# Kernel tuning notes

Hardware: AMD Instinct MI355X
Metric: run time of the kernel (lower is better)

## Reference

```python
import jax, jax.numpy as jnp
import numpy as np

NUM_HEADS = 32
HEAD_DIM = 64  # C = 3 * NUM_HEADS * HEAD_DIM = 6144
SCALE = NUM_HEADS ** (-0.5)


def setup_inputs() -> dict:
    key = jax.random.key(0)
    B, N, C = 4, 4096, 3 * NUM_HEADS * HEAD_DIM
    x = jax.random.normal(key, (B, N, C), dtype=jnp.float32)
    return {"x": x}


def reference(x):
    B, N, C = x.shape
    # (B, N, 3, H, d) -> (3, B, H, N, d)
    qkv = x.reshape(B, N, 3, NUM_HEADS, HEAD_DIM).transpose(2, 0, 3, 1, 4)
    q, k, v = qkv[0], qkv[1], qkv[2]
    q = q * SCALE
    # kv = k^T @ v : (B, H, d, d)
    kv = jnp.einsum('bhnd,bhne->bhde', k, v)
    kv = jax.nn.softmax(kv, axis=-1)  # dropout p=0.0 -> identity
    # attn = q @ kv^T : (B, H, N, d)
    attn = jnp.einsum('bhnd,bhed->bhne', q, kv)
    # (B, H, N, d) -> (B, N, H*d)
    out = attn.transpose(0, 2, 1, 3).reshape(B, N, NUM_HEADS * HEAD_DIM)
    return out
```

## Files before the change

### kernel.cpp

```cpp
#include <hip/hip_runtime.h>
#include <math.h>


#define NN 4096
#define CC 6144
#define QSCALE 0.17677669529663687f
#define NCHUNK 8

typedef __attribute__((ext_vector_type(8))) short bf16x8;
typedef __attribute__((ext_vector_type(4))) float f32x4;

static __device__ __forceinline__ unsigned short f2bf(float f) {
  unsigned u = __float_as_uint(f);
  u = (u + 0x7FFFu + ((u >> 16) & 1u)) >> 16;
  return (unsigned short)u;
}

__global__ __launch_bounds__(256, 4) void k1_kv_accum(const float* __restrict__ x,
                                                      float* __restrict__ ws1) {
  __shared__ float lds[2][4096];

  const int bid = blockIdx.x;
  const int bh = bid >> 3;
  const int chunk = bid & (NCHUNK - 1);
  const int b = bh >> 5, h = bh & 31;
  const int t = threadIdx.x;
  const int lane = t & 63;
  const int w = t >> 6;

  const long long row0 = (long long)b * NN + (long long)chunk * 512;
  const float* kbase = x + row0 * CC + 2048 + h * 64;
  const float* kl = kbase + (lane & 3) * CC + (lane >> 2) + w * 16;
  const float* vl = kl + 2048;

#define K1_STAGE(sb, bbv)                                                                 \
  do {                                                                                    \
    const float* kp_ = kl + (sb) * 32 * CC;                                               \
    const float* vp_ = vl + (sb) * 32 * CC;                                               \
    _Pragma("unroll") for (int r_ = 0; r_ < 2; ++r_)                                      \
    _Pragma("unroll") for (int sub_ = 0; sub_ < 4; ++sub_) {                              \
      const int ro_ = (sub_ * 8 + r_ * 4) * CC;                                           \
      const int li_ = w * 512 + r_ * 256 + sub_ * 64;                                     \
      __builtin_amdgcn_global_load_lds(                                                   \
          (const __attribute__((address_space(1))) void*)(kp_ + ro_),                     \
          (__attribute__((address_space(3))) void*)&lds[(bbv)][li_], 4, 0, 0);            \
      __builtin_amdgcn_global_load_lds(                                                   \
          (const __attribute__((address_space(1))) void*)(vp_ + ro_),                     \
          (__attribute__((address_space(3))) void*)&lds[(bbv)][2048 + li_], 4, 0, 0);     \
    }                                                                                     \
  } while (0)

#define K1_FRAG(bbv, baseidx, hi8, lo8)                                                   \
  do {                                                                                    \
    const float4 f0_ = *(const float4*)&lds[(bbv)][(baseidx) + lane * 4];                 \
    const float4 f1_ = *(const float4*)&lds[(bbv)][(baseidx) + 256 + lane * 4];           \
    const float ff_[8] = {f0_.x, f0_.y, f0_.z, f0_.w, f1_.x, f1_.y, f1_.z, f1_.w};        \
    _Pragma("unroll") for (int e_ = 0; e_ < 8; ++e_) {                                    \
      const unsigned u_ = __float_as_uint(ff_[e_]);                                       \
      hi8[e_] = (short)(u_ >> 16);       \
      const float lof_ = ff_[e_] - __uint_as_float(u_ & 0xFFFF0000u);                     \
      lo8[e_] = (short)(__float_as_uint(lof_) >> 16);                                     \
    }                                                                                     \
  } while (0)

  f32x4 acc[2][2];
#pragma unroll
  for (int i2 = 0; i2 < 2; ++i2)
#pragma unroll
    for (int j2 = 0; j2 < 2; ++j2) acc[i2][j2] = (f32x4){0.f, 0.f, 0.f, 0.f};

  const int mt0 = (w & 1) * 2;
  const int nt0 = (w >> 1) * 2;

  K1_STAGE(0, 0);
  asm volatile("s_waitcnt vmcnt(0)" ::: "memory");
  __syncthreads();

  for (int s = 0; s < 16; ++s) {
    const int bb = s & 1;
    if (s + 1 < 16) K1_STAGE(s + 1, bb ^ 1);

    bf16x8 ah[2], al[2], bh8[2], bl8[2];
#pragma unroll
    for (int i2 = 0; i2 < 2; ++i2) K1_FRAG(bb, (mt0 + i2) * 512, ah[i2], al[i2]);
#pragma unroll
    for (int j2 = 0; j2 < 2; ++j2) K1_FRAG(bb, 2048 + (nt0 + j2) * 512, bh8[j2], bl8[j2]);

#pragma unroll
    for (int i2 = 0; i2 < 2; ++i2)
#pragma unroll
      for (int j2 = 0; j2 < 2; ++j2) {
        acc[i2][j2] = __builtin_amdgcn_mfma_f32_16x16x32_bf16(ah[i2], bh8[j2], acc[i2][j2], 0, 0, 0);
        acc[i2][j2] = __builtin_amdgcn_mfma_f32_16x16x32_bf16(ah[i2], bl8[j2], acc[i2][j2], 0, 0, 0);
        acc[i2][j2] = __builtin_amdgcn_mfma_f32_16x16x32_bf16(al[i2], bh8[j2], acc[i2][j2], 0, 0, 0);
      }

    if (s + 1 < 16) {
      asm volatile("s_waitcnt vmcnt(0)" ::: "memory");
      __syncthreads();
    }
  }

  float* dst = ws1 + (long long)bid * 4096;
  const int g = lane >> 4, cl = lane & 15;
#pragma unroll
  for (int i2 = 0; i2 < 2; ++i2)
#pragma unroll
    for (int j2 = 0; j2 < 2; ++j2)
#pragma unroll
      for (int r = 0; r < 4; ++r)
        dst[((mt0 + i2) * 16 + g * 4 + r) * 64 + (nt0 + j2) * 16 + cl] = acc[i2][j2][r];
}

__global__ __launch_bounds__(256) void k2_softmax(const float* __restrict__ ws1,
                                                  unsigned short* __restrict__ ws2bf) {
  const int bh = blockIdx.x;
  __shared__ float Cs[64 * 65];
  __shared__ float Ss[64 * 65];
  const int t = threadIdx.x;
  const float* src = ws1 + (long long)bh * NCHUNK * 4096;
  for (int s0 = t; s0 < 1024; s0 += 256) {
    float4 sum = {0.f, 0.f, 0.f, 0.f};
#pragma unroll
    for (int c = 0; c < NCHUNK; ++c) {
      const float4 f = *(const float4*)&src[c * 4096 + s0 * 4];
      sum.x += f.x; sum.y += f.y; sum.z += f.z; sum.w += f.w;
    }
    const float se[4] = {sum.x, sum.y, sum.z, sum.w};
#pragma unroll
    for (int e = 0; e < 4; ++e) {
      const int idx = s0 * 4 + e;
      Cs[(idx >> 6) * 65 + (idx & 63)] = se[e];
    }
  }
  __syncthreads();
  if (t < 64) {
    const int a = t;
    float m = -3.0e38f;
    for (int c = 0; c < 64; ++c) m = fmaxf(m, Cs[a * 65 + c]);
    float sum = 0.f;
    for (int c = 0; c < 64; ++c) {
      const float e = expf(Cs[a * 65 + c] - m);
      Ss[a * 65 + c] = e;
      sum += e;
    }
    const float inv = QSCALE / sum;
    for (int c = 0; c < 64; ++c) Ss[a * 65 + c] *= inv;
  }
  __syncthreads();
  unsigned short* dst = ws2bf + (long long)bh * 4096;
  for (int idx = t; idx < 4096; idx += 256) {
    const int j = idx >> 6;
    const int i = idx & 63;
    dst[idx] = f2bf(Ss[j * 65 + i]);
  }
}

__global__ __launch_bounds__(256) void k3_apply(const float* __restrict__ x,
                                                const unsigned short* __restrict__ ws2bf,
                                                float* __restrict__ out) {
  const int bid = blockIdx.x;
  const int bh = bid >> 5;
  const int tile = bid & 31;
  const int b = bh >> 5, h = bh & 31;
  const int t = threadIdx.x;
  const int lane = t & 63;
  const int w = t >> 6;
  const int bn = lane & 15;
  const int g = lane >> 4;

  const unsigned short* mb = ws2bf + (long long)bh * 4096;
  bf16x8 afr[4][2];
#pragma unroll
  for (int mt = 0; mt < 4; ++mt)
#pragma unroll
    for (int kc = 0; kc < 2; ++kc)
      afr[mt][kc] = *(const bf16x8*)(mb + (mt * 16 + bn) * 64 + kc * 32 + g * 8);

  const float* qb = x + ((long long)b * NN + tile * 128) * CC + h * 64;
  bf16x8 bfr[2][2];
#pragma unroll
  for (int u = 0; u < 2; ++u) {
    const int nt = w * 2 + u;
#pragma unroll
    for (int kc = 0; kc < 2; ++kc) {
      const float* p = qb + (long long)(nt * 16 + bn) * CC + kc * 32 + g * 8;
      const float4 f0 = *(const float4*)p;
      const float4 f1 = *(const float4*)(p + 4);
      bf16x8 r;
      r[0] = (short)f2bf(f0.x); r[1] = (short)f2bf(f0.y);
      r[2] = (short)f2bf(f0.z); r[3] = (short)f2bf(f0.w);
      r[4] = (short)f2bf(f1.x); r[5] = (short)f2bf(f1.y);
      r[6] = (short)f2bf(f1.z); r[7] = (short)f2bf(f1.w);
      bfr[u][kc] = r;
    }
  }

  f32x4 acc[2][4];
#pragma unroll
  for (int u = 0; u < 2; ++u)
#pragma unroll
    for (int mt = 0; mt < 4; ++mt) acc[u][mt] = (f32x4){0.f, 0.f, 0.f, 0.f};

#pragma unroll
  for (int kc = 0; kc < 2; ++kc)
#pragma unroll
    for (int u = 0; u < 2; ++u)
#pragma unroll
      for (int mt = 0; mt < 4; ++mt)
        acc[u][mt] = __builtin_amdgcn_mfma_f32_16x16x32_bf16(afr[mt][kc], bfr[u][kc],
                                                             acc[u][mt], 0, 0, 0);

  const long long rowg = (long long)b * NN + tile * 128;
#pragma unroll
  for (int u = 0; u < 2; ++u) {
    const int nt = w * 2 + u;
    const long long r = rowg + nt * 16 + bn;
#pragma unroll
    for (int mt = 0; mt < 4; ++mt) {
      float* op = out + r * 2048 + h * 64 + mt * 16 + g * 4;
      const float4 o = {acc[u][mt][0], acc[u][mt][1], acc[u][mt][2], acc[u][mt][3]};
      *(float4*)op = o;
    }
  }
}

extern "C" void kernel_launch(void* const* d_in, const int* in_sizes, int n_in,
                              void* d_out, int out_size, void* d_ws, size_t ws_size,
                              hipStream_t stream) {
  const float* x = (const float*)d_in[0];
  float* out = (float*)d_out;
  float* ws1 = (float*)d_ws;
  unsigned short* ws2bf = (unsigned short*)(ws1 + (size_t)128 * NCHUNK * 4096);

  k1_kv_accum<<<128 * NCHUNK, 256, 0, stream>>>(x, ws1);
  k2_softmax<<<128, 256, 0, stream>>>(ws1, ws2bf);
  k3_apply<<<128 * 32, 256, 0, stream>>>(x, ws2bf, out);
}
```

Before: 148.9 us.

## Fuse softmax into kv kernel via last-block ticket and retile apply kernel

The softmax stage moves into the kv-accumulation kernel: each chunk block takes an atomic ticket, and the last block for each (b,h) reduces the partial sums, applies softmax and writes the bf16 matrix. This removes one kernel launch and its serial gap, at the cost of a memset and a tail in which 128 blocks run the softmax. The apply kernel is also retiled so each block handles 16 rows across all 32 heads, with 8 heads per wave, which gives contiguous output rows but fewer blocks (1024) and more per-thread work. Fusion only happens when the workspace is large enough to hold the counters.

```diff
diff --git a/kernel.cpp b/kernel.cpp
--- a/kernel.cpp
+++ b/kernel.cpp
@@ -16,9 +16,14 @@
   return (unsigned short)u;
 }
 
-__global__ __launch_bounds__(256, 4) void k1_kv_accum(const float* __restrict__ x,
-                                                      float* __restrict__ ws1) {
-  __shared__ float lds[2][4096];
+__global__ __launch_bounds__(256, 4) void k1_fused(const float* __restrict__ x,
+                                                   float* __restrict__ ws1,
+                                                   unsigned short* __restrict__ ws2bf,
+                                                   unsigned int* __restrict__ cnt,
+                                                   const int fused) {
+  __shared__ float smem[8320];
+  __shared__ unsigned int ticket_s;
+  float(*lds)[4096] = (float(*)[4096])smem;
 
   const int bid = blockIdx.x;
   const int bh = bid >> 3;
@@ -102,14 +107,63 @@
   }
 
   float* dst = ws1 + (long long)bid * 4096;
-  const int g = lane >> 4, cl = lane & 15;
-#pragma unroll
-  for (int i2 = 0; i2 < 2; ++i2)
-#pragma unroll
-    for (int j2 = 0; j2 < 2; ++j2)
-#pragma unroll
-      for (int r = 0; r < 4; ++r)
-        dst[((mt0 + i2) * 16 + g * 4 + r) * 64 + (nt0 + j2) * 16 + cl] = acc[i2][j2][r];
+  {
+    const int g = lane >> 4, cl = lane & 15;
+#pragma unroll
+    for (int i2 = 0; i2 < 2; ++i2)
+#pragma unroll
+      for (int j2 = 0; j2 < 2; ++j2)
+#pragma unroll
+        for (int r = 0; r < 4; ++r)
+          dst[((mt0 + i2) * 16 + g * 4 + r) * 64 + (nt0 + j2) * 16 + cl] = acc[i2][j2][r];
+  }
+
+  if (!fused) return;
+
+  __threadfence();
+  if (t == 0) ticket_s = atomicAdd(&cnt[bh], 1u);
+  __syncthreads();
+  if (ticket_s != NCHUNK - 1) return;
+  __threadfence();
+
+  float* Cs = smem;
+  float* Ss = smem + 4160;
+  const float* src = ws1 + (long long)bh * NCHUNK * 4096;
+  for (int s0 = t; s0 < 1024; s0 += 256) {
+    float4 sum = {0.f, 0.f, 0.f, 0.f};
+#pragma unroll
+    for (int c = 0; c < NCHUNK; ++c) {
+      const float4 f = *(const float4*)&src[c * 4096 + s0 * 4];
+      sum.x += f.x; sum.y += f.y; sum.z += f.z; sum.w += f.w;
+    }
+    const float se[4] = {sum.x, sum.y, sum.z, sum.w};
+#pragma unroll
+    for (int e = 0; e < 4; ++e) {
+      const int idx = s0 * 4 + e;
+      Cs[(idx >> 6) * 65 + (idx & 63)] = se[e];
+    }
+  }
+  __syncthreads();
+  if (t < 64) {
+    const int a = t;
+    float m = -3.0e38f;
+    for (int c = 0; c < 64; ++c) m = fmaxf(m, Cs[a * 65 + c]);
+    float sum = 0.f;
+    for (int c = 0; c < 64; ++c) {
+      const float e = expf(Cs[a * 65 + c] - m);
+      Ss[a * 65 + c] = e;
+      sum += e;
+    }
+    const float inv = QSCALE / sum;
+    for (int c = 0; c < 64; ++c) Ss[a * 65 + c] *= inv;
+  }
+  __syncthreads();
+  unsigned short* dstb = ws2bf + (long long)bh * 4096;
+  for (int idx = t; idx < 4096; idx += 256) {
+    const int j = idx >> 6;
+    const int i = idx & 63;
+    dstb[idx] = f2bf(Ss[j * 65 + i]);
+  }
 }
 
 __global__ __launch_bounds__(256) void k2_softmax(const float* __restrict__ ws1,
@@ -160,31 +214,35 @@
                                                 const unsigned short* __restrict__ ws2bf,
                                                 float* __restrict__ out) {
   const int bid = blockIdx.x;
-  const int bh = bid >> 5;
-  const int tile = bid & 31;
-  const int b = bh >> 5, h = bh & 31;
+  const int b = bid >> 8;
+  const int tile = bid & 255;
   const int t = threadIdx.x;
   const int lane = t & 63;
   const int w = t >> 6;
   const int bn = lane & 15;
   const int g = lane >> 4;
 
-  const unsigned short* mb = ws2bf + (long long)bh * 4096;
-  bf16x8 afr[4][2];
-#pragma unroll
-  for (int mt = 0; mt < 4; ++mt)
-#pragma unroll
-    for (int kc = 0; kc < 2; ++kc)
-      afr[mt][kc] = *(const bf16x8*)(mb + (mt * 16 + bn) * 64 + kc * 32 + g * 8);
-
-  const float* qb = x + ((long long)b * NN + tile * 128) * CC + h * 64;
-  bf16x8 bfr[2][2];
-#pragma unroll
-  for (int u = 0; u < 2; ++u) {
-    const int nt = w * 2 + u;
+  const long long row = (long long)b * NN + tile * 16 + bn;
+  const float* qrow = x + row * CC;
+  float* orow = out + row * 2048;
+  const unsigned short* sbase = ws2bf + (long long)b * 32 * 4096;
+
+#pragma unroll 2
+  for (int hh = 0; hh < 8; ++hh) {
+    const int h = w * 8 + hh;
+    const unsigned short* mb = sbase + h * 4096;
+
+    bf16x8 afr[4][2];
+#pragma unroll
+    for (int mt = 0; mt < 4; ++mt)
+#pragma unroll
+      for (int kc = 0; kc < 2; ++kc)
+        afr[mt][kc] = *(const bf16x8*)(mb + (mt * 16 + bn) * 64 + kc * 32 + g * 8);
+
+    bf16x8 bfr[2];
 #pragma unroll
     for (int kc = 0; kc < 2; ++kc) {
-      const float* p = qb + (long long)(nt * 16 + bn) * CC + kc * 32 + g * 8;
+      const float* p = qrow + h * 64 + kc * 32 + g * 8;
       const float4 f0 = *(const float4*)p;
       const float4 f1 = *(const float4*)(p + 4);
       bf16x8 r;
@@ -192,35 +250,22 @@
       r[2] = (short)f2bf(f0.z); r[3] = (short)f2bf(f0.w);
       r[4] = (short)f2bf(f1.x); r[5] = (short)f2bf(f1.y);
       r[6] = (short)f2bf(f1.z); r[7] = (short)f2bf(f1.w);
-      bfr[u][kc] = r;
-    }
-  }
-
-  f32x4 acc[2][4];
-#pragma unroll
-  for (int u = 0; u < 2; ++u)
-#pragma unroll
-    for (int mt = 0; mt < 4; ++mt) acc[u][mt] = (f32x4){0.f, 0.f, 0.f, 0.f};
-
-#pragma unroll
-  for (int kc = 0; kc < 2; ++kc)
-#pragma unroll
-    for (int u = 0; u < 2; ++u)
+      bfr[kc] = r;
+    }
+
+    f32x4 acc[4];
+#pragma unroll
+    for (int mt = 0; mt < 4; ++mt) acc[mt] = (f32x4){0.f, 0.f, 0.f, 0.f};
+#pragma unroll
+    for (int kc = 0; kc < 2; ++kc)
 #pragma unroll
       for (int mt = 0; mt < 4; ++mt)
-        acc[u][mt] = __builtin_amdgcn_mfma_f32_16x16x32_bf16(afr[mt][kc], bfr[u][kc],
-                                                             acc[u][mt], 0, 0, 0);
-
-  const long long rowg = (long long)b * NN + tile * 128;
-#pragma unroll
-  for (int u = 0; u < 2; ++u) {
-    const int nt = w * 2 + u;
-    const long long r = rowg + nt * 16 + bn;
+        acc[mt] = __builtin_amdgcn_mfma_f32_16x16x32_bf16(afr[mt][kc], bfr[kc], acc[mt], 0, 0, 0);
+
 #pragma unroll
     for (int mt = 0; mt < 4; ++mt) {
-      float* op = out + r * 2048 + h * 64 + mt * 16 + g * 4;
-      const float4 o = {acc[u][mt][0], acc[u][mt][1], acc[u][mt][2], acc[u][mt][3]};
-      *(float4*)op = o;
+      const float4 o = {acc[mt][0], acc[mt][1], acc[mt][2], acc[mt][3]};
+      *(float4*)&orow[h * 64 + mt * 16 + g * 4] = o;
     }
   }
 }
@@ -232,8 +277,16 @@
   float* out = (float*)d_out;
   float* ws1 = (float*)d_ws;
   unsigned short* ws2bf = (unsigned short*)(ws1 + (size_t)128 * NCHUNK * 4096);
-
-  k1_kv_accum<<<128 * NCHUNK, 256, 0, stream>>>(x, ws1);
-  k2_softmax<<<128, 256, 0, stream>>>(ws1, ws2bf);
-  k3_apply<<<128 * 32, 256, 0, stream>>>(x, ws2bf, out);
-}
+  const size_t base_bytes = (size_t)128 * NCHUNK * 4096 * 4 + (size_t)128 * 4096 * 2;
+  unsigned int* cnt = (unsigned int*)((char*)d_ws + base_bytes);
+  const bool can_fuse = ws_size >= base_bytes + 128 * sizeof(unsigned int);
+
+  if (can_fuse) {
+    hipMemsetAsync(cnt, 0, 128 * sizeof(unsigned int), stream);
+    k1_fused<<<128 * NCHUNK, 256, 0, stream>>>(x, ws1, ws2bf, cnt, 1);
+  } else {
+    k1_fused<<<128 * NCHUNK, 256, 0, stream>>>(x, ws1, ws2bf, cnt, 0);
+    k2_softmax<<<128, 256, 0, stream>>>(ws1, ws2bf);
+  }
+  k3_apply<<<1024, 256, 0, stream>>>(x, ws2bf, out);
+}
```

After: 394.4 us. +164.9%, slower.

## Remap apply kernel so each block covers all heads for 16 rows

Applied to the files above, without the earlier changes.

The apply kernel's work mapping changes from one block per (batch, head, 128-row tile) to one block per (batch, 16-row tile) covering all 32 heads, with each wave looping over 8 heads. Each block now reads and writes whole contiguous row segments of q and out, which should improve DRAM locality, and the grid shrinks from 4096 to 1024 blocks. In exchange, every block reloads the softmaxed kv matrix for all 32 heads, about 256KB of bf16 per block, which puts more pressure on L2. Per-wave parallelism also falls, since only one 16-row tile is in flight per head iteration.

```diff
diff --git a/kernel.cpp b/kernel.cpp
--- a/kernel.cpp
+++ b/kernel.cpp
@@ -160,31 +160,35 @@
                                                 const unsigned short* __restrict__ ws2bf,
                                                 float* __restrict__ out) {
   const int bid = blockIdx.x;
-  const int bh = bid >> 5;
-  const int tile = bid & 31;
-  const int b = bh >> 5, h = bh & 31;
+  const int b = bid >> 8;
+  const int tile = bid & 255;
   const int t = threadIdx.x;
   const int lane = t & 63;
   const int w = t >> 6;
   const int bn = lane & 15;
   const int g = lane >> 4;
 
-  const unsigned short* mb = ws2bf + (long long)bh * 4096;
-  bf16x8 afr[4][2];
-#pragma unroll
-  for (int mt = 0; mt < 4; ++mt)
-#pragma unroll
-    for (int kc = 0; kc < 2; ++kc)
-      afr[mt][kc] = *(const bf16x8*)(mb + (mt * 16 + bn) * 64 + kc * 32 + g * 8);
-
-  const float* qb = x + ((long long)b * NN + tile * 128) * CC + h * 64;
-  bf16x8 bfr[2][2];
-#pragma unroll
-  for (int u = 0; u < 2; ++u) {
-    const int nt = w * 2 + u;
+  const long long row = (long long)b * NN + tile * 16 + bn;
+  const float* qrow = x + row * CC;
+  float* orow = out + row * 2048;
+  const unsigned short* sbase = ws2bf + (long long)b * 32 * 4096;
+
+#pragma unroll 2
+  for (int hh = 0; hh < 8; ++hh) {
+    const int h = w * 8 + hh;
+    const unsigned short* mb = sbase + h * 4096;
+
+    bf16x8 afr[4][2];
+#pragma unroll
+    for (int mt = 0; mt < 4; ++mt)
+#pragma unroll
+      for (int kc = 0; kc < 2; ++kc)
+        afr[mt][kc] = *(const bf16x8*)(mb + (mt * 16 + bn) * 64 + kc * 32 + g * 8);
+
+    bf16x8 bfr[2];
 #pragma unroll
     for (int kc = 0; kc < 2; ++kc) {
-      const float* p = qb + (long long)(nt * 16 + bn) * CC + kc * 32 + g * 8;
+      const float* p = qrow + h * 64 + kc * 32 + g * 8;
       const float4 f0 = *(const float4*)p;
       const float4 f1 = *(const float4*)(p + 4);
       bf16x8 r;
@@ -192,35 +196,22 @@
       r[2] = (short)f2bf(f0.z); r[3] = (short)f2bf(f0.w);
       r[4] = (short)f2bf(f1.x); r[5] = (short)f2bf(f1.y);
       r[6] = (short)f2bf(f1.z); r[7] = (short)f2bf(f1.w);
-      bfr[u][kc] = r;
-    }
-  }
-
-  f32x4 acc[2][4];
-#pragma unroll
-  for (int u = 0; u < 2; ++u)
-#pragma unroll
-    for (int mt = 0; mt < 4; ++mt) acc[u][mt] = (f32x4){0.f, 0.f, 0.f, 0.f};
-
-#pragma unroll
-  for (int kc = 0; kc < 2; ++kc)
-#pragma unroll
-    for (int u = 0; u < 2; ++u)
+      bfr[kc] = r;
+    }
+
+    f32x4 acc[4];
+#pragma unroll
+    for (int mt = 0; mt < 4; ++mt) acc[mt] = (f32x4){0.f, 0.f, 0.f, 0.f};
+#pragma unroll
+    for (int kc = 0; kc < 2; ++kc)
 #pragma unroll
       for (int mt = 0; mt < 4; ++mt)
-        acc[u][mt] = __builtin_amdgcn_mfma_f32_16x16x32_bf16(afr[mt][kc], bfr[u][kc],
-                                                             acc[u][mt], 0, 0, 0);
-
-  const long long rowg = (long long)b * NN + tile * 128;
-#pragma unroll
-  for (int u = 0; u < 2; ++u) {
-    const int nt = w * 2 + u;
-    const long long r = rowg + nt * 16 + bn;
+        acc[mt] = __builtin_amdgcn_mfma_f32_16x16x32_bf16(afr[mt][kc], bfr[kc], acc[mt], 0, 0, 0);
+
 #pragma unroll
     for (int mt = 0; mt < 4; ++mt) {
-      float* op = out + r * 2048 + h * 64 + mt * 16 + g * 4;
-      const float4 o = {acc[u][mt][0], acc[u][mt][1], acc[u][mt][2], acc[u][mt][3]};
-      *(float4*)op = o;
+      const float4 o = {acc[mt][0], acc[mt][1], acc[mt][2], acc[mt][3]};
+      *(float4*)&orow[h * 64 + mt * 16 + g * 4] = o;
     }
   }
 }
@@ -235,5 +226,5 @@
 
   k1_kv_accum<<<128 * NCHUNK, 256, 0, stream>>>(x, ws1);
   k2_softmax<<<128, 256, 0, stream>>>(ws1, ws2bf);
-  k3_apply<<<128 * 32, 256, 0, stream>>>(x, ws2bf, out);
-}
+  k3_apply<<<1024, 256, 0, stream>>>(x, ws2bf, out);
+}
```

New measurement: 160.6 us. 1.08x slower.
